# Performance work log

Measured on AMD Instinct MI355X. Metric: run time of the kernel, lower is better.

The kernel has to match this reference:

```python
import jax, jax.numpy as jnp
import numpy as np

N = 16384            # number of input vectors
CODEBOOK_SIZE = 8192  # M
DIM = 256             # dim_feature
BETA = 0.25           # commitment_weight


def setup_inputs() -> dict:
    key = jax.random.key(0)
    kx, ke = jax.random.split(key)
    x = jax.random.normal(kx, (N, DIM), dtype=jnp.float32)
    # kaiming-uniform-style init for the codebook
    bound = float(np.sqrt(3.0 / DIM))
    embeddings = jax.random.uniform(ke, (CODEBOOK_SIZE, DIM), dtype=jnp.float32,
                                    minval=-bound, maxval=bound)
    return {"x": x, "embeddings": embeddings}


def reference(x, embeddings):
    # l2_dist: sqrt(sum((x_i - e_j)^2)) computed via the GEMM expansion
    x2 = jnp.sum(x * x, axis=1, keepdims=True)               # (N, 1)
    e2 = jnp.sum(embeddings * embeddings, axis=1)            # (M,)
    d2 = x2 + e2[None, :] - 2.0 * (x @ embeddings.T)         # (N, M)
    dist = jnp.sqrt(jnp.maximum(d2, 0.0))
    # deterministic gumbel_sample path (training eval / stochastic=False):
    # argmax of logits = -dist  <=>  argmin of dist
    ind = jnp.argmin(dist, axis=1)                           # (N,)
    quantized = embeddings[ind]                              # one_hot @ embeddings
    # commitment loss: beta * ||x_q - sg(x)||^2 (docstring)
    commit_loss = BETA * jnp.mean((quantized - jax.lax.stop_gradient(x)) ** 2)
    # straight-through estimator
    quantized_st = x + jax.lax.stop_gradient(quantized - x)
    # perplexity from per-code counts (one-hot scatter)
    counts = jnp.zeros((CODEBOOK_SIZE,), jnp.float32).at[ind].add(1.0)
    probs = counts / counts.sum()
    perplexity = jnp.exp(-jnp.sum(probs * jnp.log(probs + 1e-10)))
    return quantized_st, ind, commit_loss, perplexity
```

## Files before the change

### kernel.cpp

```cpp
#include <hip/hip_runtime.h>
#include <stdint.h>


#define N_VEC 16384
#define M_CODES 8192
#define DIM 256
#define BETA 0.25f

#define NSLICE 8
#define SLICE_CODES 1024
#define BM 256
#define BN 128
#define BK 32
#define NPART 16
#define STEP_BYTES 49152
#define RING_BYTES (3 * STEP_BYTES)
#define LDS_TOTAL (RING_BYTES + 4096)
#define NSTEPS 64

typedef __attribute__((ext_vector_type(4))) float f32x4;
typedef __attribute__((ext_vector_type(8))) __bf16 bf16x8;

__device__ __forceinline__ void gll16(const void* g, const void* lds_p) {
    __builtin_amdgcn_global_load_lds(
        (const __attribute__((address_space(1))) uint32_t*)(uintptr_t)g,
        (__attribute__((address_space(3))) uint32_t*)(uint32_t)(uintptr_t)lds_p,
        16, 0, 0);
}

__device__ __forceinline__ ushort f2bf(float f) {
    uint32_t u = __float_as_uint(f);
    return (ushort)((u + 0x7FFFu + ((u >> 16) & 1u)) >> 16);
}
__device__ __forceinline__ float bf2f(ushort h) {
    return __uint_as_float(((uint32_t)h) << 16);
}

__global__ __launch_bounds__(256) void prep_kernel(
    const float* __restrict__ x, const float* __restrict__ emb,
    ushort* __restrict__ xh, ushort* __restrict__ xl,
    ushort* __restrict__ eh, ushort* __restrict__ el,
    float* __restrict__ e2, unsigned* __restrict__ counts,
    float* __restrict__ loss_acc) {
    if (blockIdx.x < 8) {
        int4 z = {0, 0, 0, 0};
        ((int4*)counts)[blockIdx.x * 256 + threadIdx.x] = z;
        if (blockIdx.x == 0 && threadIdx.x == 0) *loss_acc = 0.0f;
    }
    const int wave = threadIdx.x >> 6;
    const int lane = threadIdx.x & 63;
    const int row = blockIdx.x * 4 + wave;

    const float* src;
    ushort* ph;
    ushort* pl;
    bool is_e;
    int er = row - N_VEC;
    if (row < N_VEC) {
        src = x + (size_t)row * DIM;
        ph = xh + (size_t)row * DIM;
        pl = xl + (size_t)row * DIM;
        is_e = false;
    } else {
        src = emb + (size_t)er * DIM;
        ph = eh + (size_t)er * DIM;
        pl = el + (size_t)er * DIM;
        is_e = true;
    }
    float4 v = *(const float4*)(src + lane * 4);
    ushort h0 = f2bf(v.x), h1 = f2bf(v.y), h2 = f2bf(v.z), h3 = f2bf(v.w);
    ushort l0 = f2bf(v.x - bf2f(h0)), l1 = f2bf(v.y - bf2f(h1));
    ushort l2 = f2bf(v.z - bf2f(h2)), l3 = f2bf(v.w - bf2f(h3));
    *(ushort4*)(ph + lane * 4) = make_ushort4(h0, h1, h2, h3);
    *(ushort4*)(pl + lane * 4) = make_ushort4(l0, l1, l2, l3);
    if (is_e) {
        float s = v.x * v.x + v.y * v.y + v.z * v.z + v.w * v.w;
        #pragma unroll
        for (int off = 32; off; off >>= 1) s += __shfl_xor(s, off);
        if (lane == 0) e2[er] = s;
    }
}

__global__ __launch_bounds__(512, 2) void vq_mfma_kernel(
    const ushort* __restrict__ xh, const ushort* __restrict__ xl,
    const ushort* __restrict__ eh, const ushort* __restrict__ el,
    const float* __restrict__ e2g, unsigned long long* __restrict__ partials) {
    extern __shared__ char lds[];

    const int t = threadIdx.x;
    const int lane = t & 63;
    const int wv = t >> 6;
    const int lane15 = lane & 15;
    const int l16 = lane >> 4;

    const int slice = blockIdx.x & 7;
    const int rt = blockIdx.x >> 3;
    const int row0 = rt * BM;
    const int cslice0 = slice * SLICE_CODES;

    const int wr0 = (wv & 3) * 64;
    const int wc0 = (wv >> 2) * 64;

    int byteA[4], byteB[4];
    #pragma unroll
    for (int f = 0; f < 4; ++f) {
        int ra = wr0 + f * 16 + lane15;
        byteA[f] = ra * 64 + (((l16 ^ (ra >> 1)) & 3) << 4);
        int rb = wc0 + f * 16 + lane15;
        byteB[f] = rb * 64 + (((l16 ^ (rb >> 1)) & 3) << 4);
    }

    const int r_a = t >> 2;
    const int c_a = ((t & 3) ^ ((t >> 3) & 3));
    const ushort* pxh_a = xh + (size_t)(row0 + r_a) * DIM + c_a * 8;
    const ushort* pxh_b = pxh_a + (size_t)128 * DIM;
    const ushort* pxl_a = xl + (size_t)(row0 + r_a) * DIM + c_a * 8;
    const ushort* pxl_b = pxl_a + (size_t)128 * DIM;
    const ushort* peh = eh + (size_t)(cslice0 + r_a) * DIM + c_a * 8;
    const ushort* pel = el + (size_t)(cslice0 + r_a) * DIM + c_a * 8;

    float* e2s = (float*)(lds + RING_BYTES);
    e2s[t] = e2g[cslice0 + t];
    e2s[t + 512] = e2g[cslice0 + t + 512];
    asm volatile("s_waitcnt lgkmcnt(0)" ::: "memory");

    float best[16];
    int bidx[16];
    #pragma unroll
    for (int s = 0; s < 16; ++s) { best[s] = __uint_as_float(0x7f800000u); bidx[s] = 0; }

    f32x4 acc[4][4];
    #pragma unroll
    for (int fi = 0; fi < 4; ++fi)
        #pragma unroll
        for (int fj = 0; fj < 4; ++fj) acc[fi][fj] = (f32x4){0.f, 0.f, 0.f, 0.f};

    auto stage = [&](int sidx) {
        const int ct = sidx >> 3;
        const int kc = sidx & 7;
        char* base = lds + (sidx % 3) * STEP_BYTES + wv * 1024;
        const int xo = kc * 32;
        const size_t eo = ((size_t)ct << 15) + xo;
        gll16(pxh_a + xo, base);
        gll16(pxh_b + xo, base + 8192);
        gll16(pxl_a + xo, base + 16384);
        gll16(pxl_b + xo, base + 24576);
        gll16(peh + eo, base + 32768);
        gll16(pel + eo, base + 40960);
    };

    auto compute = [&](int sidx) {
        const char* lb = lds + (sidx % 3) * STEP_BYTES;
        bf16x8 ah[4], alo[4], bh[4], blo[4];
        #pragma unroll
        for (int f = 0; f < 4; ++f) {
            ah[f] = *(const bf16x8*)(lb + byteA[f]);
            alo[f] = *(const bf16x8*)(lb + 16384 + byteA[f]);
            bh[f] = *(const bf16x8*)(lb + 32768 + byteB[f]);
            blo[f] = *(const bf16x8*)(lb + 40960 + byteB[f]);
        }
        __builtin_amdgcn_s_setprio(1);
        #pragma unroll
        for (int fi = 0; fi < 4; ++fi)
            #pragma unroll
            for (int fj = 0; fj < 4; ++fj)
                acc[fi][fj] = __builtin_amdgcn_mfma_f32_16x16x32_bf16(
                    ah[fi], bh[fj], acc[fi][fj], 0, 0, 0);
        #pragma unroll
        for (int fi = 0; fi < 4; ++fi)
            #pragma unroll
            for (int fj = 0; fj < 4; ++fj)
                acc[fi][fj] = __builtin_amdgcn_mfma_f32_16x16x32_bf16(
                    ah[fi], blo[fj], acc[fi][fj], 0, 0, 0);
        #pragma unroll
        for (int fi = 0; fi < 4; ++fi)
            #pragma unroll
            for (int fj = 0; fj < 4; ++fj)
                acc[fi][fj] = __builtin_amdgcn_mfma_f32_16x16x32_bf16(
                    alo[fi], bh[fj], acc[fi][fj], 0, 0, 0);
        __builtin_amdgcn_s_setprio(0);

        if ((sidx & 7) == 7) {
            const int ct = sidx >> 3;
            const int cb = cslice0 + ct * BN + wc0;
            #pragma unroll
            for (int fj = 0; fj < 4; ++fj) {
                const int cl = ct * BN + wc0 + fj * 16 + lane15;
                const float e2v = e2s[cl];
                const int c = cb + fj * 16 + lane15;
                #pragma unroll
                for (int fi = 0; fi < 4; ++fi)
                    #pragma unroll
                    for (int r = 0; r < 4; ++r) {
                        float sc = e2v - 2.0f * acc[fi][fj][r];
                        const int slot = fi * 4 + r;
                        if (sc < best[slot]) { best[slot] = sc; bidx[slot] = c; }
                    }
            }
            #pragma unroll
            for (int fi = 0; fi < 4; ++fi)
                #pragma unroll
                for (int fj = 0; fj < 4; ++fj) acc[fi][fj] = (f32x4){0.f, 0.f, 0.f, 0.f};
        }
    };

    stage(0);
    stage(1);

    for (int sidx = 0; sidx < NSTEPS - 1; ++sidx) {
        asm volatile("s_waitcnt vmcnt(6)" ::: "memory");
        __builtin_amdgcn_s_barrier();
        if (sidx < NSTEPS - 2) stage(sidx + 2);
        compute(sidx);
    }
    asm volatile("s_waitcnt vmcnt(0)" ::: "memory");
    __builtin_amdgcn_s_barrier();
    compute(NSTEPS - 1);

    #pragma unroll
    for (int slot = 0; slot < 16; ++slot) {
        float v = best[slot];
        int ix = bidx[slot];
        #pragma unroll
        for (int off = 1; off < 16; off <<= 1) {
            float v2 = __shfl_xor(v, off);
            int ix2 = __shfl_xor(ix, off);
            if (v2 < v || (v2 == v && ix2 < ix)) { v = v2; ix = ix2; }
        }
        if (lane15 == 0) {
            int fi = slot >> 2, r = slot & 3;
            int row = row0 + wr0 + fi * 16 + l16 * 4 + r;
            uint32_t u = __float_as_uint(v);
            uint32_t ord = (u & 0x80000000u) ? ~u : (u | 0x80000000u);
            partials[(size_t)(slice * 2 + (wv >> 2)) * N_VEC + row] =
                ((unsigned long long)ord << 32) | (unsigned)ix;
        }
    }
}

__global__ __launch_bounds__(256) void finish_kernel(
    const float* __restrict__ x, const float* __restrict__ emb,
    const unsigned long long* __restrict__ partials,
    float* __restrict__ out_ind, float* __restrict__ out_q,
    unsigned* __restrict__ counts, float* __restrict__ loss_acc) {
    __shared__ float partial[4];
    const int wave = threadIdx.x >> 6;
    const int lane = threadIdx.x & 63;
    const int row = blockIdx.x * 4 + wave;

    unsigned long long m = ~0ull;
    if (lane < NPART) m = partials[(size_t)lane * N_VEC + row];
    #pragma unroll
    for (int off = 1; off < NPART; off <<= 1) {
        unsigned long long v = __shfl_xor(m, off);
        if (v < m) m = v;
    }
    m = __shfl(m, 0);
    const int ix = (int)(unsigned)(m & 0xFFFFFFFFull);

    float4 q = *(const float4*)(emb + (size_t)ix * DIM + lane * 4);
    float4 xv = *(const float4*)(x + (size_t)row * DIM + lane * 4);
    *(float4*)(out_q + (size_t)row * DIM + lane * 4) = q;
    float dx = q.x - xv.x, dy = q.y - xv.y, dz = q.z - xv.z, dw = q.w - xv.w;
    float s = dx * dx + dy * dy + dz * dz + dw * dw;
    #pragma unroll
    for (int off = 32; off; off >>= 1) s += __shfl_xor(s, off);
    if (lane == 0) {
        out_ind[row] = (float)ix;
        atomicAdd(&counts[ix], 1u);
        partial[wave] = s;
    }
    __syncthreads();
    if (threadIdx.x == 0)
        atomicAdd(loss_acc, partial[0] + partial[1] + partial[2] + partial[3]);
}

__global__ __launch_bounds__(256) void finalize_kernel(
    const unsigned* __restrict__ counts, const float* __restrict__ loss_acc,
    float* __restrict__ out_scalars) {
    __shared__ float red[256];
    float h = 0.0f;
    for (int c = threadIdx.x; c < M_CODES; c += 256) {
        float p = (float)counts[c] * (1.0f / (float)N_VEC);
        h += p * logf(p + 1e-10f);
    }
    red[threadIdx.x] = h;
    __syncthreads();
    for (int s = 128; s; s >>= 1) {
        if (threadIdx.x < s) red[threadIdx.x] += red[threadIdx.x + s];
        __syncthreads();
    }
    if (threadIdx.x == 0) {
        out_scalars[0] = BETA * loss_acc[0] / (float)(N_VEC * DIM);
        out_scalars[1] = expf(-red[0]);
    }
}

extern "C" void kernel_launch(void* const* d_in, const int* in_sizes, int n_in,
                              void* d_out, int out_size, void* d_ws, size_t ws_size,
                              hipStream_t stream) {
    const float* x = (const float*)d_in[0];
    const float* emb = (const float*)d_in[1];

    float* out = (float*)d_out;
    float* out_q = out;
    float* out_ind = out + (size_t)N_VEC * DIM;
    float* out_scalars = out_ind + N_VEC;

    ushort* xh = (ushort*)out;
    ushort* xl = xh + (size_t)N_VEC * DIM;

    char* wp = (char*)d_ws;
    ushort* eh = (ushort*)wp;  wp += (size_t)M_CODES * DIM * 2;
    ushort* el = (ushort*)wp;  wp += (size_t)M_CODES * DIM * 2;
    float* e2 = (float*)wp;    wp += (size_t)M_CODES * 4;
    unsigned long long* partials = (unsigned long long*)wp;
    wp += (size_t)NPART * N_VEC * 8;
    unsigned* counts = (unsigned*)wp; wp += (size_t)M_CODES * 4;
    float* loss_acc = (float*)wp;

    prep_kernel<<<(N_VEC + M_CODES) / 4, 256, 0, stream>>>(x, emb, xh, xl, eh, el,
                                                           e2, counts, loss_acc);

    hipFuncSetAttribute((const void*)vq_mfma_kernel,
                        hipFuncAttributeMaxDynamicSharedMemorySize, LDS_TOTAL);
    vq_mfma_kernel<<<(N_VEC / BM) * NSLICE, 512, LDS_TOTAL, stream>>>(
        xh, xl, eh, el, e2, partials);

    finish_kernel<<<N_VEC / 4, 256, 0, stream>>>(x, emb, partials, out_ind, out_q,
                                                 counts, loss_acc);
    finalize_kernel<<<1, 256, 0, stream>>>(counts, loss_acc, out_scalars);
}
```

Baseline: 271.6 us.

## Widen codebook tile to 256 and split LDS ring into X double-buffer and E triple-buffer

Raises the code tile per block from 128 to 256 columns, so the x tile is reused across twice as many codes and each wave holds a 64x128 accumulator (4x8 fragments). The LDS staging is split into a double-buffered X region and a triple-buffered E region with per-step vmcnt accounting, and e2 is loaded from global into registers instead of going through LDS. The block index mapping changes so row tiles vary fastest, and the slice count halves. The cost is double the accumulator registers, which may squeeze occupancy at launch bounds (512,2), plus a larger LDS footprint.

```diff
diff --git a/kernel.cpp b/kernel.cpp
--- a/kernel.cpp
+++ b/kernel.cpp
@@ -7,15 +7,16 @@
 #define DIM 256
 #define BETA 0.25f
 
-#define NSLICE 8
-#define SLICE_CODES 1024
+#define NSLICE 4
+#define SLICE_CODES 2048
 #define BM 256
-#define BN 128
-#define BK 32
-#define NPART 16
-#define STEP_BYTES 49152
-#define RING_BYTES (3 * STEP_BYTES)
-#define LDS_TOTAL (RING_BYTES + 4096)
+#define BN 256
+#define NPART 8
+
+#define XSLOT 32768
+#define ESLOT 32768
+#define EBASE (2 * XSLOT)
+#define LDS_TOTAL (2 * XSLOT + 3 * ESLOT)
 #define NSTEPS 64
 
 typedef __attribute__((ext_vector_type(4))) float f32x4;
@@ -27,6 +28,7 @@
         (__attribute__((address_space(3))) uint32_t*)(uint32_t)(uintptr_t)lds_p,
         16, 0, 0);
 }
+#define SB0() __builtin_amdgcn_sched_barrier(0)
 
 __device__ __forceinline__ ushort f2bf(float f) {
     uint32_t u = __float_as_uint(f);
@@ -93,129 +95,149 @@
     const int lane15 = lane & 15;
     const int l16 = lane >> 4;
 
-    const int slice = blockIdx.x & 7;
-    const int rt = blockIdx.x >> 3;
+    const int rt = blockIdx.x & 63;
+    const int slice = blockIdx.x >> 6;
     const int row0 = rt * BM;
     const int cslice0 = slice * SLICE_CODES;
 
     const int wr0 = (wv & 3) * 64;
-    const int wc0 = (wv >> 2) * 64;
-
-    int byteA[4], byteB[4];
+    const int wch = wv >> 2;
+
+    int byteA[4], byteB[8];
     #pragma unroll
     for (int f = 0; f < 4; ++f) {
         int ra = wr0 + f * 16 + lane15;
         byteA[f] = ra * 64 + (((l16 ^ (ra >> 1)) & 3) << 4);
-        int rb = wc0 + f * 16 + lane15;
+    }
+    #pragma unroll
+    for (int f = 0; f < 8; ++f) {
+        int rb = wch * 128 + f * 16 + lane15;
         byteB[f] = rb * 64 + (((l16 ^ (rb >> 1)) & 3) << 4);
     }
 
-    const int r_a = t >> 2;
-    const int c_a = ((t & 3) ^ ((t >> 3) & 3));
-    const ushort* pxh_a = xh + (size_t)(row0 + r_a) * DIM + c_a * 8;
-    const ushort* pxh_b = pxh_a + (size_t)128 * DIM;
-    const ushort* pxl_a = xl + (size_t)(row0 + r_a) * DIM + c_a * 8;
-    const ushort* pxl_b = pxl_a + (size_t)128 * DIM;
-    const ushort* peh = eh + (size_t)(cslice0 + r_a) * DIM + c_a * 8;
-    const ushort* pel = el + (size_t)(cslice0 + r_a) * DIM + c_a * 8;
-
-    float* e2s = (float*)(lds + RING_BYTES);
-    e2s[t] = e2g[cslice0 + t];
-    e2s[t + 512] = e2g[cslice0 + t + 512];
-    asm volatile("s_waitcnt lgkmcnt(0)" ::: "memory");
+    const int s0 = wv * 128 + lane;
+    const int s1 = s0 + 64;
+    const int r0s = s0 >> 2, r1s = s1 >> 2;
+    const int c0s = ((s0 & 3) ^ ((s0 >> 3) & 3)) << 3;
+    const int c1s = ((s1 & 3) ^ ((s1 >> 3) & 3)) << 3;
+    const ushort* pxh_a = xh + (size_t)(row0 + r0s) * DIM + c0s;
+    const ushort* pxh_b = xh + (size_t)(row0 + r1s) * DIM + c1s;
+    const ushort* pxl_a = xl + (size_t)(row0 + r0s) * DIM + c0s;
+    const ushort* pxl_b = xl + (size_t)(row0 + r1s) * DIM + c1s;
+    const ushort* peh_a = eh + (size_t)(cslice0 + r0s) * DIM + c0s;
+    const ushort* peh_b = eh + (size_t)(cslice0 + r1s) * DIM + c1s;
+    const ushort* pel_a = el + (size_t)(cslice0 + r0s) * DIM + c0s;
+    const ushort* pel_b = el + (size_t)(cslice0 + r1s) * DIM + c1s;
+    const int wdst = wv * 2048;
+
+    auto stage_X = [&](int s) {
+        char* b = lds + (s & 1) * XSLOT + wdst;
+        const int xo = (s & 7) * 32;
+        gll16(pxh_a + xo, b);
+        gll16(pxh_b + xo, b + 1024);
+        gll16(pxl_a + xo, b + 16384);
+        gll16(pxl_b + xo, b + 16384 + 1024);
+    };
+    auto stage_E = [&](int slot, int s) {
+        char* b = lds + EBASE + slot * ESLOT + wdst;
+        const size_t eo = ((size_t)(s >> 3) << 16) + (s & 7) * 32;
+        gll16(peh_a + eo, b);
+        gll16(peh_b + eo, b + 1024);
+        gll16(pel_a + eo, b + 16384);
+        gll16(pel_b + eo, b + 16384 + 1024);
+    };
 
     float best[16];
     int bidx[16];
     #pragma unroll
     for (int s = 0; s < 16; ++s) { best[s] = __uint_as_float(0x7f800000u); bidx[s] = 0; }
 
-    f32x4 acc[4][4];
+    f32x4 acc[4][8];
     #pragma unroll
     for (int fi = 0; fi < 4; ++fi)
         #pragma unroll
-        for (int fj = 0; fj < 4; ++fj) acc[fi][fj] = (f32x4){0.f, 0.f, 0.f, 0.f};
-
-    auto stage = [&](int sidx) {
-        const int ct = sidx >> 3;
-        const int kc = sidx & 7;
-        char* base = lds + (sidx % 3) * STEP_BYTES + wv * 1024;
-        const int xo = kc * 32;
-        const size_t eo = ((size_t)ct << 15) + xo;
-        gll16(pxh_a + xo, base);
-        gll16(pxh_b + xo, base + 8192);
-        gll16(pxl_a + xo, base + 16384);
-        gll16(pxl_b + xo, base + 24576);
-        gll16(peh + eo, base + 32768);
-        gll16(pel + eo, base + 40960);
-    };
-
-    auto compute = [&](int sidx) {
-        const char* lb = lds + (sidx % 3) * STEP_BYTES;
-        bf16x8 ah[4], alo[4], bh[4], blo[4];
+        for (int fj = 0; fj < 8; ++fj) acc[fi][fj] = (f32x4){0.f, 0.f, 0.f, 0.f};
+
+    stage_X(0); SB0();
+    stage_E(0, 0); SB0();
+    stage_E(1, 1); SB0();
+
+    int esl = 0;
+    for (int ct = 0; ct < 8; ++ct) {
+        float e2r[8];
         #pragma unroll
-        for (int f = 0; f < 4; ++f) {
-            ah[f] = *(const bf16x8*)(lb + byteA[f]);
-            alo[f] = *(const bf16x8*)(lb + 16384 + byteA[f]);
-            bh[f] = *(const bf16x8*)(lb + 32768 + byteB[f]);
-            blo[f] = *(const bf16x8*)(lb + 40960 + byteB[f]);
-        }
-        __builtin_amdgcn_s_setprio(1);
-        #pragma unroll
-        for (int fi = 0; fi < 4; ++fi)
+        for (int kc = 0; kc < 8; ++kc) {
+            const int s = ct * 8 + kc;
+            if (kc == 1) {
+                asm volatile("s_waitcnt vmcnt(12)" ::: "memory");
+            } else if (kc == 7 && ct == 7) {
+                asm volatile("s_waitcnt vmcnt(0)" ::: "memory");
+            } else {
+                asm volatile("s_waitcnt vmcnt(4)" ::: "memory");
+            }
+            __builtin_amdgcn_s_barrier();
+            SB0();
+            if (s + 1 < NSTEPS) { stage_X(s + 1); SB0(); }
+            const int stslot = (esl >= 1) ? esl - 1 : 2;
+            if (s + 2 < NSTEPS) { stage_E(stslot, s + 2); SB0(); }
+            if (kc == 0) {
+                #pragma unroll
+                for (int fj = 0; fj < 8; ++fj)
+                    e2r[fj] = e2g[cslice0 + ct * BN + wch * 128 + fj * 16 + lane15];
+                SB0();
+            }
+
+            const char* lbX = lds + (s & 1) * XSLOT;
+            const char* lbE = lds + EBASE + esl * ESLOT;
+            bf16x8 ah[4], alo[4];
             #pragma unroll
-            for (int fj = 0; fj < 4; ++fj)
-                acc[fi][fj] = __builtin_amdgcn_mfma_f32_16x16x32_bf16(
-                    ah[fi], bh[fj], acc[fi][fj], 0, 0, 0);
-        #pragma unroll
-        for (int fi = 0; fi < 4; ++fi)
+            for (int f = 0; f < 4; ++f) {
+                ah[f] = *(const bf16x8*)(lbX + byteA[f]);
+                alo[f] = *(const bf16x8*)(lbX + 16384 + byteA[f]);
+            }
+            __builtin_amdgcn_s_setprio(1);
             #pragma unroll
-            for (int fj = 0; fj < 4; ++fj)
-                acc[fi][fj] = __builtin_amdgcn_mfma_f32_16x16x32_bf16(
-                    ah[fi], blo[fj], acc[fi][fj], 0, 0, 0);
-        #pragma unroll
-        for (int fi = 0; fi < 4; ++fi)
-            #pragma unroll
-            for (int fj = 0; fj < 4; ++fj)
-                acc[fi][fj] = __builtin_amdgcn_mfma_f32_16x16x32_bf16(
-                    alo[fi], bh[fj], acc[fi][fj], 0, 0, 0);
-        __builtin_amdgcn_s_setprio(0);
-
-        if ((sidx & 7) == 7) {
-            const int ct = sidx >> 3;
-            const int cb = cslice0 + ct * BN + wc0;
-            #pragma unroll
-            for (int fj = 0; fj < 4; ++fj) {
-                const int cl = ct * BN + wc0 + fj * 16 + lane15;
-                const float e2v = e2s[cl];
-                const int c = cb + fj * 16 + lane15;
+            for (int fj = 0; fj < 8; ++fj) {
+                bf16x8 bh = *(const bf16x8*)(lbE + byteB[fj]);
+                bf16x8 blo = *(const bf16x8*)(lbE + 16384 + byteB[fj]);
+                #pragma unroll
+                for (int fi = 0; fi < 4; ++fi)
+                    acc[fi][fj] = __builtin_amdgcn_mfma_f32_16x16x32_bf16(
+                        ah[fi], bh, acc[fi][fj], 0, 0, 0);
+                #pragma unroll
+                for (int fi = 0; fi < 4; ++fi)
+                    acc[fi][fj] = __builtin_amdgcn_mfma_f32_16x16x32_bf16(
+                        ah[fi], blo, acc[fi][fj], 0, 0, 0);
+                #pragma unroll
+                for (int fi = 0; fi < 4; ++fi)
+                    acc[fi][fj] = __builtin_amdgcn_mfma_f32_16x16x32_bf16(
+                        alo[fi], bh, acc[fi][fj], 0, 0, 0);
+            }
+            __builtin_amdgcn_s_setprio(0);
+            esl = (esl == 2) ? 0 : esl + 1;
+
+            if (kc == 7) {
+                const int cb = cslice0 + ct * BN + wch * 128;
+                #pragma unroll
+                for (int fj = 0; fj < 8; ++fj) {
+                    const int c = cb + fj * 16 + lane15;
+                    #pragma unroll
+                    for (int fi = 0; fi < 4; ++fi)
+                        #pragma unroll
+                        for (int r = 0; r < 4; ++r) {
+                            float sc = e2r[fj] - 2.0f * acc[fi][fj][r];
+                            const int slot = fi * 4 + r;
+                            if (sc < best[slot]) { best[slot] = sc; bidx[slot] = c; }
+                        }
+                }
                 #pragma unroll
                 for (int fi = 0; fi < 4; ++fi)
                     #pragma unroll
-                    for (int r = 0; r < 4; ++r) {
-                        float sc = e2v - 2.0f * acc[fi][fj][r];
-                        const int slot = fi * 4 + r;
-                        if (sc < best[slot]) { best[slot] = sc; bidx[slot] = c; }
-                    }
-            }
-            #pragma unroll
-            for (int fi = 0; fi < 4; ++fi)
-                #pragma unroll
-                for (int fj = 0; fj < 4; ++fj) acc[fi][fj] = (f32x4){0.f, 0.f, 0.f, 0.f};
+                    for (int fj = 0; fj < 8; ++fj)
+                        acc[fi][fj] = (f32x4){0.f, 0.f, 0.f, 0.f};
+            }
         }
-    };
-
-    stage(0);
-    stage(1);
-
-    for (int sidx = 0; sidx < NSTEPS - 1; ++sidx) {
-        asm volatile("s_waitcnt vmcnt(6)" ::: "memory");
-        __builtin_amdgcn_s_barrier();
-        if (sidx < NSTEPS - 2) stage(sidx + 2);
-        compute(sidx);
-    }
-    asm volatile("s_waitcnt vmcnt(0)" ::: "memory");
-    __builtin_amdgcn_s_barrier();
-    compute(NSTEPS - 1);
+    }
 
     #pragma unroll
     for (int slot = 0; slot < 16; ++slot) {
@@ -232,7 +254,7 @@
             int row = row0 + wr0 + fi * 16 + l16 * 4 + r;
             uint32_t u = __float_as_uint(v);
             uint32_t ord = (u & 0x80000000u) ? ~u : (u | 0x80000000u);
-            partials[(size_t)(slice * 2 + (wv >> 2)) * N_VEC + row] =
+            partials[(size_t)(slice * 2 + wch) * N_VEC + row] =
                 ((unsigned long long)ord << 32) | (unsigned)ix;
         }
     }
```

After: 334.5 us. +23.2%, slower.
